# Performance work log

Hardware: AMD Instinct MI355X
Metric: run time of the kernel (lower is better)

The kernel has to match this reference:

```python
import jax, jax.numpy as jnp
import numpy as np

VOC, EDIM, HDIM, SSZ, SDIM, SDEPTH, NACT = 32000, 256, 256, 64, 64, 2, 3
T, B = 256, 128
PAD = 0


def setup_inputs() -> dict:
    key = jax.random.key(0)
    ks = jax.random.split(key, 20)
    s = 0.1
    inp = {
        'inputs': jax.random.randint(ks[0], (T, B), 0, VOC, dtype=jnp.int64) if jax.config.jax_enable_x64 else jax.random.randint(ks[0], (T, B), 0, VOC, dtype=jnp.int32),
        'emb_W': (jax.random.normal(ks[1], (VOC, EDIM)) * s).at[PAD].set(0.0),
        'W_hh': jax.random.normal(ks[2], (HDIM, HDIM)) * s,
        'b_hh': jnp.zeros((HDIM,)),
        'W_eh': jax.random.normal(ks[3], (HDIM, EDIM)) * s,
        'b_eh': jnp.zeros((HDIM,)),
        'W_ha': jax.random.normal(ks[4], (NACT, HDIM)) * s,
        'b_ha': jnp.zeros((NACT,)),
        'W_hg': jax.random.normal(ks[5], (1, HDIM)) * s,
        'b_hg': jnp.zeros((1,)),
        'W_hs': jax.random.normal(ks[6], (SDIM, HDIM)) * s,
        'b_hs': jnp.zeros((SDIM,)),
        'W_sh': jax.random.normal(ks[7], (HDIM, SDIM * SDEPTH)) * s,
        'b_sh': jnp.zeros((HDIM,)),
        'W_su': jax.random.normal(ks[8], (SDIM, SDIM * SDEPTH)) * s,
        'b_su': jnp.zeros((SDIM,)),
        'empty_elem': jax.random.normal(ks[9], (1, SDIM)) * s,
    }
    return inp


def _shift_down(s):  # W_down @ s : row i <- row i-1, row 0 <- 0  (push)
    return jnp.concatenate([jnp.zeros_like(s[:, :1]), s[:, :-1]], axis=1)


def _shift_up(s, k):  # (W_up)^k @ s : row i <- row i+k, tail rows <- 0 (pop)
    return jnp.concatenate([s[:, k:], jnp.zeros_like(s[:, :k])], axis=1)


def reference(inputs, emb_W, W_hh, b_hh, W_eh, b_eh, W_ha, b_ha, W_hg, b_hg,
              W_hs, b_hs, W_sh, b_sh, W_su, b_su, empty_elem):
    bsz = inputs.shape[1]
    embs = emb_W[inputs]                               # [T, B, EDIM]
    hid0 = jnp.zeros((bsz, HDIM), embs.dtype)
    stack0 = jnp.broadcast_to(empty_elem, (bsz, SSZ, SDIM))

    def step(carry, emb):
        hid, stack = carry
        tops = stack[:, :SDEPTH].reshape(bsz, SDEPTH * SDIM)
        mhid = emb @ W_eh.T + b_eh + hid @ W_hh.T + b_hh + tops @ W_sh.T + b_sh
        act_logits = hid @ W_ha.T + b_ha               # [B, 3]
        gamma = 1.0 + jax.nn.softplus(hid @ W_hg.T + b_hg)  # [B, 1]
        act = jax.nn.softmax(act_logits, axis=-1)
        sharp = act ** gamma
        sharp = sharp / (jnp.sum(sharp, axis=-1, keepdims=True) + 1e-16)
        act_chosen = jnp.argmax(sharp, axis=-1)        # topk(k=1)
        p_push = sharp[:, 0][:, None, None]
        p_pop = sharp[:, 1][:, None, None]
        p_noop = sharp[:, 2][:, None, None]
        push_val = jax.nn.relu(hid @ W_hs.T + b_hs)    # [B, SDIM]
        u_val = jax.nn.relu(tops @ W_su.T + b_su)      # [B, SDIM]
        stack_push = _shift_down(stack).at[:, 0].add(push_val)
        stack_pop = _shift_down(_shift_up(stack, SDEPTH)).at[:, 0].add(u_val)
        new_stack = p_push * stack_push + p_pop * stack_pop + p_noop * stack
        new_hid = jax.nn.relu(mhid)
        return (new_hid, new_stack), (new_hid, act_chosen)

    (hid, stack), (outputs, acts) = jax.lax.scan(step, (hid0, stack0), embs)
    return outputs, hid, stack, acts
```

## Files before the change

### kernel.cpp

```cpp
#include <hip/hip_runtime.h>

#define T_STEPS 256
#define BATCH 128

#define WEHT_OFF 0
#define WHHT_OFF 65536
#define WSHT_OFF 131072
#define WHST_OFF 163840
#define WSUT_OFF 180224
#define BC_OFF   188416

#define HID_OFF   8388608
#define STACK_OFF 8421376
#define ACTS_OFF  8945664

#define BAR_LDS() do { \
    asm volatile("s_waitcnt lgkmcnt(0)" ::: "memory"); \
    __builtin_amdgcn_s_barrier(); \
} while (0)

__device__ __forceinline__ float rl(float v, int l) {
    return __int_as_float(__builtin_amdgcn_readlane(__float_as_int(v), l));
}

__global__ __launch_bounds__(256) void prep_kernel(
    const float* __restrict__ W_hh, const float* __restrict__ b_hh,
    const float* __restrict__ W_eh, const float* __restrict__ b_eh,
    const float* __restrict__ W_sh, const float* __restrict__ b_sh,
    const float* __restrict__ W_hs, const float* __restrict__ W_su,
    float* __restrict__ ws)
{
    int idx = blockIdx.x * 256 + threadIdx.x;
    if (idx < 65536) {
        ws[WEHT_OFF + idx] = W_eh[(idx & 255) * 256 + (idx >> 8)];
    } else if (idx < 131072) {
        int k = idx - 65536;
        ws[WHHT_OFF + k] = W_hh[(k & 255) * 256 + (k >> 8)];
    } else if (idx < 163840) {
        int k = idx - 131072;
        ws[WSHT_OFF + k] = W_sh[(k & 255) * 128 + (k >> 8)];
    } else if (idx < 180224) {
        int k = idx - 163840;
        ws[WHST_OFF + k] = W_hs[(k & 63) * 256 + (k >> 6)];
    } else if (idx < 188416) {
        int k = idx - 180224;
        ws[WSUT_OFF + k] = W_su[(k & 63) * 128 + (k >> 6)];
    } else if (idx < 188672) {
        int k = idx - 188416;
        ws[BC_OFF + k] = b_eh[k] + b_hh[k] + b_sh[k];
    }
}

__global__ __launch_bounds__(256) void ex_gemm(
    const int* __restrict__ tokens, const float* __restrict__ emb_W,
    const float* __restrict__ ws, float* __restrict__ outp)
{
    __shared__ __align__(16) float aT[64 * 40];
    __shared__ int tok[32];
    const int t = threadIdx.x;
    const int rg = t >> 6;
    const int c0 = (t & 63) * 4;
    const int R0 = blockIdx.x * 32;
    if (t < 32) tok[t] = tokens[R0 + t];
    __syncthreads();

    float acc[8][4];
#pragma unroll
    for (int r = 0; r < 8; r++)
#pragma unroll
        for (int c = 0; c < 4; c++) acc[r][c] = 0.f;

    for (int e0 = 0; e0 < 256; e0 += 64) {
        {
            int r = t >> 3, seg = t & 7;
            const float* src = emb_W + (size_t)tok[r] * 256 + e0 + seg * 8;
            float4 v0 = *(const float4*)(src);
            float4 v1 = *(const float4*)(src + 4);
            int eb = seg * 8;
            aT[(eb + 0) * 40 + r] = v0.x; aT[(eb + 1) * 40 + r] = v0.y;
            aT[(eb + 2) * 40 + r] = v0.z; aT[(eb + 3) * 40 + r] = v0.w;
            aT[(eb + 4) * 40 + r] = v1.x; aT[(eb + 5) * 40 + r] = v1.y;
            aT[(eb + 6) * 40 + r] = v1.z; aT[(eb + 7) * 40 + r] = v1.w;
        }
        __syncthreads();
        const float* wp = ws + WEHT_OFF + (size_t)e0 * 256 + c0;
#pragma unroll 2
        for (int e = 0; e < 64; e++) {
            float4 wv = *(const float4*)(wp + (size_t)e * 256);
            const float* ar = &aT[e * 40 + rg * 8];
            float4 a0 = *(const float4*)(ar);
            float4 a1 = *(const float4*)(ar + 4);
            acc[0][0] = fmaf(a0.x, wv.x, acc[0][0]); acc[0][1] = fmaf(a0.x, wv.y, acc[0][1]);
            acc[0][2] = fmaf(a0.x, wv.z, acc[0][2]); acc[0][3] = fmaf(a0.x, wv.w, acc[0][3]);
            acc[1][0] = fmaf(a0.y, wv.x, acc[1][0]); acc[1][1] = fmaf(a0.y, wv.y, acc[1][1]);
            acc[1][2] = fmaf(a0.y, wv.z, acc[1][2]); acc[1][3] = fmaf(a0.y, wv.w, acc[1][3]);
            acc[2][0] = fmaf(a0.z, wv.x, acc[2][0]); acc[2][1] = fmaf(a0.z, wv.y, acc[2][1]);
            acc[2][2] = fmaf(a0.z, wv.z, acc[2][2]); acc[2][3] = fmaf(a0.z, wv.w, acc[2][3]);
            acc[3][0] = fmaf(a0.w, wv.x, acc[3][0]); acc[3][1] = fmaf(a0.w, wv.y, acc[3][1]);
            acc[3][2] = fmaf(a0.w, wv.z, acc[3][2]); acc[3][3] = fmaf(a0.w, wv.w, acc[3][3]);
            acc[4][0] = fmaf(a1.x, wv.x, acc[4][0]); acc[4][1] = fmaf(a1.x, wv.y, acc[4][1]);
            acc[4][2] = fmaf(a1.x, wv.z, acc[4][2]); acc[4][3] = fmaf(a1.x, wv.w, acc[4][3]);
            acc[5][0] = fmaf(a1.y, wv.x, acc[5][0]); acc[5][1] = fmaf(a1.y, wv.y, acc[5][1]);
            acc[5][2] = fmaf(a1.y, wv.z, acc[5][2]); acc[5][3] = fmaf(a1.y, wv.w, acc[5][3]);
            acc[6][0] = fmaf(a1.z, wv.x, acc[6][0]); acc[6][1] = fmaf(a1.z, wv.y, acc[6][1]);
            acc[6][2] = fmaf(a1.z, wv.z, acc[6][2]); acc[6][3] = fmaf(a1.z, wv.w, acc[6][3]);
            acc[7][0] = fmaf(a1.w, wv.x, acc[7][0]); acc[7][1] = fmaf(a1.w, wv.y, acc[7][1]);
            acc[7][2] = fmaf(a1.w, wv.z, acc[7][2]); acc[7][3] = fmaf(a1.w, wv.w, acc[7][3]);
        }
        __syncthreads();
    }
    float4 bc4 = *(const float4*)&ws[BC_OFF + c0];
#pragma unroll
    for (int r = 0; r < 8; r++) {
        float4 o;
        o.x = acc[r][0] + bc4.x; o.y = acc[r][1] + bc4.y;
        o.z = acc[r][2] + bc4.z; o.w = acc[r][3] + bc4.w;
        *(float4*)&outp[(size_t)(R0 + rg * 8 + r) * 256 + c0] = o;
    }
}

__attribute__((amdgpu_flat_work_group_size(512, 512)))
__attribute__((amdgpu_waves_per_eu(2, 2)))
__global__ void rnn_scan(
    const float* __restrict__ ws,
    const float* __restrict__ W_ha, const float* __restrict__ b_ha,
    const float* __restrict__ W_hg, const float* __restrict__ b_hg,
    const float* __restrict__ b_hs, const float* __restrict__ b_su,
    const float* __restrict__ empty_elem,
    float* __restrict__ out)
{
    __shared__ __align__(16) float hid[256];
    __shared__ __align__(16) float tops[128];
    __shared__ __align__(16) float partial[8 * 256];
    __shared__ __align__(16) float2 pp2[8 * 64];
    __shared__ __align__(16) float bnd[16 * 64];
    __shared__ __align__(16) float wsu_l[8192];
    __shared__ __align__(16) float whs_l[16384];
    __shared__ __align__(16) float whaL[1024];
    __shared__ __align__(16) float scal[4];

    const int t = threadIdx.x, lane = t & 63, w = t >> 6;
    const int b = blockIdx.x;

    float4 whh[32], wsh[16];
    {
        const float* base = ws + WHHT_OFF + (size_t)(w * 32) * 256 + lane * 4;
#pragma unroll
        for (int e = 0; e < 32; e++) whh[e] = *(const float4*)(base + (size_t)e * 256);
        const float* base2 = ws + WSHT_OFF + (size_t)(w * 16) * 256 + lane * 4;
#pragma unroll
        for (int j = 0; j < 16; j++) wsh[j] = *(const float4*)(base2 + (size_t)j * 256);
    }
#pragma unroll
    for (int e = 0; e < 32; e++)
        asm volatile("" : "+v"(whh[e].x), "+v"(whh[e].y), "+v"(whh[e].z), "+v"(whh[e].w));
#pragma unroll
    for (int j = 0; j < 16; j++)
        asm volatile("" : "+v"(wsh[j].x), "+v"(wsh[j].y), "+v"(wsh[j].z), "+v"(wsh[j].w));

    float bscal = 0.f;
    if (lane == 0 && w < 4) bscal = (w < 3) ? b_ha[w] : b_hg[0];
    float bhs_r = 0.f, bsu_r = 0.f;
    if (w == 0) { bhs_r = b_hs[lane]; bsu_r = b_su[lane]; }

    const float ev = empty_elem[lane];
    float sv[8];
#pragma unroll
    for (int k = 0; k < 8; k++) sv[k] = ev;
    if (t < 256) hid[t] = 0.f;
    if (t < 128) tops[t] = empty_elem[t & 63];
    bnd[(w * 2) * 64 + lane] = ev;
    bnd[(w * 2 + 1) * 64 + lane] = ev;
    for (int i = t; i < 16384; i += 512)
        whs_l[(i >> 8) * 256 + (i & 63) * 4 + ((i >> 6) & 3)] = ws[WHST_OFF + i];
    for (int i = t; i < 8192; i += 512) {
        int j = i >> 6, s = i & 63;
        wsu_l[(j >> 2) * 256 + s * 4 + (j & 3)] = ws[WSUT_OFF + i];
    }
    for (int i = t; i < 1024; i += 512)
        whaL[i] = (i < 768) ? W_ha[i] : W_hg[i - 768];
    __syncthreads();

    const float* slice_ptr = (lane < 32) ? &hid[w * 32 + lane]
                                         : &tops[w * 16 + (lane & 15)];

    float exv = (w >= 4) ? out[(size_t)b * 256 + (t - 256)] : 0.f;

    const float4* whs4 = (const float4*)whs_l;
    const float4* wsu4 = (const float4*)wsu_l;

    for (int ts = 0; ts < T_STEPS; ts++) {
        float exn = 0.f;
        if (w >= 4 && ts + 1 < T_STEPS)
            exn = out[((size_t)(ts + 1) * BATCH + b) * 256 + (t - 256)];

        float halo_lo = (w == 0) ? 0.f : bnd[((w - 1) * 2 + 1) * 64 + lane];
        float halo_hi = (w == 7) ? 0.f : bnd[((w + 1) * 2) * 64 + lane];

        float slice = *slice_ptr;
        float4 acc = make_float4(0.f, 0.f, 0.f, 0.f);
        float accP = 0.f, accU = 0.f;
#pragma unroll
        for (int eb = 0; eb < 8; eb++) {
            float4 sp = whs4[(w * 8 + eb) * 64 + lane];
            float h0 = rl(slice, 4 * eb + 0);
            float h1 = rl(slice, 4 * eb + 1);
            float h2 = rl(slice, 4 * eb + 2);
            float h3 = rl(slice, 4 * eb + 3);
            acc.x = fmaf(whh[eb*4+0].x, h0, acc.x);
            acc.y = fmaf(whh[eb*4+0].y, h0, acc.y);
            acc.z = fmaf(whh[eb*4+0].z, h0, acc.z);
            acc.w = fmaf(whh[eb*4+0].w, h0, acc.w);
            acc.x = fmaf(whh[eb*4+1].x, h1, acc.x);
            acc.y = fmaf(whh[eb*4+1].y, h1, acc.y);
            acc.z = fmaf(whh[eb*4+1].z, h1, acc.z);
            acc.w = fmaf(whh[eb*4+1].w, h1, acc.w);
            acc.x = fmaf(whh[eb*4+2].x, h2, acc.x);
            acc.y = fmaf(whh[eb*4+2].y, h2, acc.y);
            acc.z = fmaf(whh[eb*4+2].z, h2, acc.z);
            acc.w = fmaf(whh[eb*4+2].w, h2, acc.w);
            acc.x = fmaf(whh[eb*4+3].x, h3, acc.x);
            acc.y = fmaf(whh[eb*4+3].y, h3, acc.y);
            acc.z = fmaf(whh[eb*4+3].z, h3, acc.z);
            acc.w = fmaf(whh[eb*4+3].w, h3, acc.w);
            accP = fmaf(sp.x, h0, accP);
            accP = fmaf(sp.y, h1, accP);
            accP = fmaf(sp.z, h2, accP);
            accP = fmaf(sp.w, h3, accP);
        }
#pragma unroll
        for (int jb = 0; jb < 4; jb++) {
            float4 su = wsu4[(w * 4 + jb) * 64 + lane];
            float tv0 = rl(slice, 32 + 4 * jb);
            float tv1 = rl(slice, 32 + 4 * jb + 1);
            float tv2 = rl(slice, 32 + 4 * jb + 2);
            float tv3 = rl(slice, 32 + 4 * jb + 3);
            acc.x = fmaf(wsh[jb*4+0].x, tv0, acc.x);
            acc.y = fmaf(wsh[jb*4+0].y, tv0, acc.y);
            acc.z = fmaf(wsh[jb*4+0].z, tv0, acc.z);
            acc.w = fmaf(wsh[jb*4+0].w, tv0, acc.w);
            acc.x = fmaf(wsh[jb*4+1].x, tv1, acc.x);
            acc.y = fmaf(wsh[jb*4+1].y, tv1, acc.y);
            acc.z = fmaf(wsh[jb*4+1].z, tv1, acc.z);
            acc.w = fmaf(wsh[jb*4+1].w, tv1, acc.w);
            acc.x = fmaf(wsh[jb*4+2].x, tv2, acc.x);
            acc.y = fmaf(wsh[jb*4+2].y, tv2, acc.y);
            acc.z = fmaf(wsh[jb*4+2].z, tv2, acc.z);
            acc.w = fmaf(wsh[jb*4+2].w, tv2, acc.w);
            acc.x = fmaf(wsh[jb*4+3].x, tv3, acc.x);
            acc.y = fmaf(wsh[jb*4+3].y, tv3, acc.y);
            acc.z = fmaf(wsh[jb*4+3].z, tv3, acc.z);
            acc.w = fmaf(wsh[jb*4+3].w, tv3, acc.w);
            accU = fmaf(su.x, tv0, accU);
            accU = fmaf(su.y, tv1, accU);
            accU = fmaf(su.z, tv2, accU);
            accU = fmaf(su.w, tv3, accU);
        }
        *(float4*)&partial[w * 256 + lane * 4] = acc;
        pp2[w * 64 + lane] = make_float2(accP, accU);

        if (w < 4) {
            float bd = 0.f;
#pragma unroll
            for (int k = 0; k < 4; k++)
                bd = fmaf(whaL[w * 256 + k * 64 + lane], hid[k * 64 + lane], bd);
#pragma unroll
            for (int off = 32; off > 0; off >>= 1) bd += __shfl_down(bd, off);
            if (lane == 0) scal[w] = bd + bscal;
        }
        BAR_LDS();

        float pvv = 0.f, uvv = 0.f;
        if (w == 0) {
            float v1 = bhs_r, v2 = bsu_r;
#pragma unroll
            for (int q = 0; q < 8; q++) {
                float2 pq = pp2[q * 64 + lane];
                v1 += pq.x; v2 += pq.y;
            }
            pvv = fmaxf(v1, 0.f);
            uvv = fmaxf(v2, 0.f);
        }

        if (w >= 4) {
            int h = t - 256;
            float mh = exv;
#pragma unroll
            for (int q = 0; q < 8; q++) mh += partial[q * 256 + h];
            float nh = fmaxf(mh, 0.f);
            hid[h] = nh;
            out[((size_t)ts * BATCH + b) * 256 + h] = nh;
        }

        float4 sc4 = *(const float4*)scal;
        float l0 = sc4.x, l1 = sc4.y, l2 = sc4.z, gv = sc4.w;
        float eg = __expf(gv);
        float g = 1.f + ((gv > 15.f) ? gv : __logf(1.f + eg));
        float m = fmaxf(l0, fmaxf(l1, l2));
        float z = __expf(l0 - m) + __expf(l1 - m) + __expf(l2 - m);
        float lz = __logf(z);
        float s0  = __expf(g * (l0 - m - lz));
        float s1v = __expf(g * (l1 - m - lz));
        float s2v = __expf(g * (l2 - m - lz));
        float S = s0 + s1v + s2v + 1e-16f;
        float rS = __builtin_amdgcn_rcpf(S);
        float p0 = s0 * rS, p1 = s1v * rS, p2 = s2v * rS;

        if (t == 0) {
            int am = 0; float bm = s0;
            if (s1v > bm) { bm = s1v; am = 1; }
            if (s2v > bm) { bm = s2v; am = 2; }
            out[ACTS_OFF + ts * BATCH + b] = (float)am;
        }

        {
            float nv[8];
            float below0 = (w == 0) ? pvv : halo_lo;
            float pop0   = (w == 0) ? uvv : sv[1];
            nv[0] = fmaf(p0, below0, fmaf(p1, pop0, p2 * sv[0]));
#pragma unroll
            for (int k = 1; k < 7; k++)
                nv[k] = fmaf(p0, sv[k - 1], fmaf(p1, sv[k + 1], p2 * sv[k]));
            nv[7] = fmaf(p0, sv[6], fmaf(p1, halo_hi, p2 * sv[7]));
#pragma unroll
            for (int k = 0; k < 8; k++) sv[k] = nv[k];
        }
        bnd[(w * 2) * 64 + lane] = sv[0];
        bnd[(w * 2 + 1) * 64 + lane] = sv[7];
        if (w == 0) { tops[lane] = sv[0]; tops[64 + lane] = sv[1]; }

        exv = exn;
        BAR_LDS();
    }

    if (t < 256) out[HID_OFF + (size_t)b * 256 + t] = hid[t];
#pragma unroll
    for (int k = 0; k < 8; k++)
        out[STACK_OFF + (size_t)b * 4096 + (w * 8 + k) * 64 + lane] = sv[k];
}

extern "C" void kernel_launch(void* const* d_in, const int* in_sizes, int n_in,
                              void* d_out, int out_size, void* d_ws, size_t ws_size,
                              hipStream_t stream)
{
    (void)in_sizes; (void)n_in; (void)out_size; (void)ws_size;
    const int*   inputs     = (const int*)d_in[0];
    const float* emb_W      = (const float*)d_in[1];
    const float* W_hh       = (const float*)d_in[2];
    const float* b_hh       = (const float*)d_in[3];
    const float* W_eh       = (const float*)d_in[4];
    const float* b_eh       = (const float*)d_in[5];
    const float* W_ha       = (const float*)d_in[6];
    const float* b_ha       = (const float*)d_in[7];
    const float* W_hg       = (const float*)d_in[8];
    const float* b_hg       = (const float*)d_in[9];
    const float* W_hs       = (const float*)d_in[10];
    const float* b_hs       = (const float*)d_in[11];
    const float* W_sh       = (const float*)d_in[12];
    const float* b_sh       = (const float*)d_in[13];
    const float* W_su       = (const float*)d_in[14];
    const float* b_su       = (const float*)d_in[15];
    const float* empty_elem = (const float*)d_in[16];
    float* out = (float*)d_out;
    float* ws  = (float*)d_ws;

    hipLaunchKernelGGL(prep_kernel, dim3(737), dim3(256), 0, stream,
                       W_hh, b_hh, W_eh, b_eh, W_sh, b_sh, W_hs, W_su, ws);
    hipLaunchKernelGGL(ex_gemm, dim3(1024), dim3(256), 0, stream,
                       inputs, emb_W, ws, out);
    hipLaunchKernelGGL(rnn_scan, dim3(128), dim3(512), 0, stream,
                       ws, W_ha, b_ha, W_hg, b_hg, b_hs, b_su, empty_elem, out);
}
```

Measured before the change: 593.9 us.

## Use packed FMA in scan matvec and readlane-broadcast embeddings in ex_gemm

The recurrent matvec in rnn_scan now keeps its weights as float2 vectors and uses two-wide elementwise FMA, so the compiler can emit v_pk_fma_f32 and halve the FMA instruction count on the serial critical path. ex_gemm drops its LDS transpose staging and barriers: each lane loads one embedding element per row, values are broadcast with readlane, and the accumulation also uses packed FMA. The inner loop is fully unrolled, which raises code size and register pressure. The readlane broadcasts add scalar-path traffic in exchange for removing LDS traffic.

```diff
diff --git a/kernel.cpp b/kernel.cpp
--- a/kernel.cpp
+++ b/kernel.cpp
@@ -13,6 +13,8 @@
 #define HID_OFF   8388608
 #define STACK_OFF 8421376
 #define ACTS_OFF  8945664
+
+typedef __attribute__((ext_vector_type(2))) float f32x2;
 
 #define BAR_LDS() do { \
     asm volatile("s_waitcnt lgkmcnt(0)" ::: "memory"); \
@@ -55,66 +57,48 @@
     const int* __restrict__ tokens, const float* __restrict__ emb_W,
     const float* __restrict__ ws, float* __restrict__ outp)
 {
-    __shared__ __align__(16) float aT[64 * 40];
     __shared__ int tok[32];
-    const int t = threadIdx.x;
-    const int rg = t >> 6;
-    const int c0 = (t & 63) * 4;
+    const int t = threadIdx.x, lane = t & 63, rg = t >> 6;
+    const int c0 = lane * 4;
     const int R0 = blockIdx.x * 32;
     if (t < 32) tok[t] = tokens[R0 + t];
     __syncthreads();
-
-    float acc[8][4];
-#pragma unroll
-    for (int r = 0; r < 8; r++)
-#pragma unroll
-        for (int c = 0; c < 4; c++) acc[r][c] = 0.f;
+    int tr[8];
+#pragma unroll
+    for (int r = 0; r < 8; r++) tr[r] = tok[rg * 8 + r];
+
+    f32x2 accA[8], accB[8];
+#pragma unroll
+    for (int r = 0; r < 8; r++) {
+        accA[r] = (f32x2){0.f, 0.f};
+        accB[r] = (f32x2){0.f, 0.f};
+    }
 
     for (int e0 = 0; e0 < 256; e0 += 64) {
-        {
-            int r = t >> 3, seg = t & 7;
-            const float* src = emb_W + (size_t)tok[r] * 256 + e0 + seg * 8;
-            float4 v0 = *(const float4*)(src);
-            float4 v1 = *(const float4*)(src + 4);
-            int eb = seg * 8;
-            aT[(eb + 0) * 40 + r] = v0.x; aT[(eb + 1) * 40 + r] = v0.y;
-            aT[(eb + 2) * 40 + r] = v0.z; aT[(eb + 3) * 40 + r] = v0.w;
-            aT[(eb + 4) * 40 + r] = v1.x; aT[(eb + 5) * 40 + r] = v1.y;
-            aT[(eb + 6) * 40 + r] = v1.z; aT[(eb + 7) * 40 + r] = v1.w;
-        }
-        __syncthreads();
+        float er[8];
+#pragma unroll
+        for (int r = 0; r < 8; r++)
+            er[r] = emb_W[(size_t)tr[r] * 256 + e0 + lane];
         const float* wp = ws + WEHT_OFF + (size_t)e0 * 256 + c0;
-#pragma unroll 2
+#pragma unroll
         for (int e = 0; e < 64; e++) {
             float4 wv = *(const float4*)(wp + (size_t)e * 256);
-            const float* ar = &aT[e * 40 + rg * 8];
-            float4 a0 = *(const float4*)(ar);
-            float4 a1 = *(const float4*)(ar + 4);
-            acc[0][0] = fmaf(a0.x, wv.x, acc[0][0]); acc[0][1] = fmaf(a0.x, wv.y, acc[0][1]);
-            acc[0][2] = fmaf(a0.x, wv.z, acc[0][2]); acc[0][3] = fmaf(a0.x, wv.w, acc[0][3]);
-            acc[1][0] = fmaf(a0.y, wv.x, acc[1][0]); acc[1][1] = fmaf(a0.y, wv.y, acc[1][1]);
-            acc[1][2] = fmaf(a0.y, wv.z, acc[1][2]); acc[1][3] = fmaf(a0.y, wv.w, acc[1][3]);
-            acc[2][0] = fmaf(a0.z, wv.x, acc[2][0]); acc[2][1] = fmaf(a0.z, wv.y, acc[2][1]);
-            acc[2][2] = fmaf(a0.z, wv.z, acc[2][2]); acc[2][3] = fmaf(a0.z, wv.w, acc[2][3]);
-            acc[3][0] = fmaf(a0.w, wv.x, acc[3][0]); acc[3][1] = fmaf(a0.w, wv.y, acc[3][1]);
-            acc[3][2] = fmaf(a0.w, wv.z, acc[3][2]); acc[3][3] = fmaf(a0.w, wv.w, acc[3][3]);
-            acc[4][0] = fmaf(a1.x, wv.x, acc[4][0]); acc[4][1] = fmaf(a1.x, wv.y, acc[4][1]);
-            acc[4][2] = fmaf(a1.x, wv.z, acc[4][2]); acc[4][3] = fmaf(a1.x, wv.w, acc[4][3]);
-            acc[5][0] = fmaf(a1.y, wv.x, acc[5][0]); acc[5][1] = fmaf(a1.y, wv.y, acc[5][1]);
-            acc[5][2] = fmaf(a1.y, wv.z, acc[5][2]); acc[5][3] = fmaf(a1.y, wv.w, acc[5][3]);
-            acc[6][0] = fmaf(a1.z, wv.x, acc[6][0]); acc[6][1] = fmaf(a1.z, wv.y, acc[6][1]);
-            acc[6][2] = fmaf(a1.z, wv.z, acc[6][2]); acc[6][3] = fmaf(a1.z, wv.w, acc[6][3]);
-            acc[7][0] = fmaf(a1.w, wv.x, acc[7][0]); acc[7][1] = fmaf(a1.w, wv.y, acc[7][1]);
-            acc[7][2] = fmaf(a1.w, wv.z, acc[7][2]); acc[7][3] = fmaf(a1.w, wv.w, acc[7][3]);
-        }
-        __syncthreads();
+            f32x2 w01 = {wv.x, wv.y}, w23 = {wv.z, wv.w};
+#pragma unroll
+            for (int r = 0; r < 8; r++) {
+                float a = rl(er[r], e);
+                f32x2 av = {a, a};
+                accA[r] = __builtin_elementwise_fma(w01, av, accA[r]);
+                accB[r] = __builtin_elementwise_fma(w23, av, accB[r]);
+            }
+        }
     }
     float4 bc4 = *(const float4*)&ws[BC_OFF + c0];
 #pragma unroll
     for (int r = 0; r < 8; r++) {
         float4 o;
-        o.x = acc[r][0] + bc4.x; o.y = acc[r][1] + bc4.y;
-        o.z = acc[r][2] + bc4.z; o.w = acc[r][3] + bc4.w;
+        o.x = accA[r].x + bc4.x; o.y = accA[r].y + bc4.y;
+        o.z = accB[r].x + bc4.z; o.w = accB[r].y + bc4.w;
         *(float4*)&outp[(size_t)(R0 + rg * 8 + r) * 256 + c0] = o;
     }
 }
@@ -142,21 +126,27 @@
     const int t = threadIdx.x, lane = t & 63, w = t >> 6;
     const int b = blockIdx.x;
 
-    float4 whh[32], wsh[16];
+    f32x2 whh2[64], wsh2[32];
     {
         const float* base = ws + WHHT_OFF + (size_t)(w * 32) * 256 + lane * 4;
 #pragma unroll
-        for (int e = 0; e < 32; e++) whh[e] = *(const float4*)(base + (size_t)e * 256);
+        for (int e = 0; e < 32; e++) {
+            float4 v = *(const float4*)(base + (size_t)e * 256);
+            whh2[2 * e]     = (f32x2){v.x, v.y};
+            whh2[2 * e + 1] = (f32x2){v.z, v.w};
+        }
         const float* base2 = ws + WSHT_OFF + (size_t)(w * 16) * 256 + lane * 4;
 #pragma unroll
-        for (int j = 0; j < 16; j++) wsh[j] = *(const float4*)(base2 + (size_t)j * 256);
-    }
-#pragma unroll
-    for (int e = 0; e < 32; e++)
-        asm volatile("" : "+v"(whh[e].x), "+v"(whh[e].y), "+v"(whh[e].z), "+v"(whh[e].w));
-#pragma unroll
-    for (int j = 0; j < 16; j++)
-        asm volatile("" : "+v"(wsh[j].x), "+v"(wsh[j].y), "+v"(wsh[j].z), "+v"(wsh[j].w));
+        for (int j = 0; j < 16; j++) {
+            float4 v = *(const float4*)(base2 + (size_t)j * 256);
+            wsh2[2 * j]     = (f32x2){v.x, v.y};
+            wsh2[2 * j + 1] = (f32x2){v.z, v.w};
+        }
+    }
+#pragma unroll
+    for (int i = 0; i < 64; i++) asm volatile("" : "+v"(whh2[i]));
+#pragma unroll
+    for (int i = 0; i < 32; i++) asm volatile("" : "+v"(wsh2[i]));
 
     float bscal = 0.f;
     if (lane == 0 && w < 4) bscal = (w < 3) ? b_ha[w] : b_hg[0];
@@ -198,7 +188,7 @@
         float halo_hi = (w == 7) ? 0.f : bnd[((w + 1) * 2) * 64 + lane];
 
         float slice = *slice_ptr;
-        float4 acc = make_float4(0.f, 0.f, 0.f, 0.f);
+        f32x2 acc01 = (f32x2){0.f, 0.f}, acc23 = (f32x2){0.f, 0.f};
         float accP = 0.f, accU = 0.f;
 #pragma unroll
         for (int eb = 0; eb < 8; eb++) {
@@ -207,22 +197,15 @@
             float h1 = rl(slice, 4 * eb + 1);
             float h2 = rl(slice, 4 * eb + 2);
             float h3 = rl(slice, 4 * eb + 3);
-            acc.x = fmaf(whh[eb*4+0].x, h0, acc.x);
-            acc.y = fmaf(whh[eb*4+0].y, h0, acc.y);
-            acc.z = fmaf(whh[eb*4+0].z, h0, acc.z);
-            acc.w = fmaf(whh[eb*4+0].w, h0, acc.w);
-            acc.x = fmaf(whh[eb*4+1].x, h1, acc.x);
-            acc.y = fmaf(whh[eb*4+1].y, h1, acc.y);
-            acc.z = fmaf(whh[eb*4+1].z, h1, acc.z);
-            acc.w = fmaf(whh[eb*4+1].w, h1, acc.w);
-            acc.x = fmaf(whh[eb*4+2].x, h2, acc.x);
-            acc.y = fmaf(whh[eb*4+2].y, h2, acc.y);
-            acc.z = fmaf(whh[eb*4+2].z, h2, acc.z);
-            acc.w = fmaf(whh[eb*4+2].w, h2, acc.w);
-            acc.x = fmaf(whh[eb*4+3].x, h3, acc.x);
-            acc.y = fmaf(whh[eb*4+3].y, h3, acc.y);
-            acc.z = fmaf(whh[eb*4+3].z, h3, acc.z);
-            acc.w = fmaf(whh[eb*4+3].w, h3, acc.w);
+            f32x2 h0v = {h0, h0}, h1v = {h1, h1}, h2v = {h2, h2}, h3v = {h3, h3};
+            acc01 = __builtin_elementwise_fma(whh2[(4*eb+0)*2],   h0v, acc01);
+            acc23 = __builtin_elementwise_fma(whh2[(4*eb+0)*2+1], h0v, acc23);
+            acc01 = __builtin_elementwise_fma(whh2[(4*eb+1)*2],   h1v, acc01);
+            acc23 = __builtin_elementwise_fma(whh2[(4*eb+1)*2+1], h1v, acc23);
+            acc01 = __builtin_elementwise_fma(whh2[(4*eb+2)*2],   h2v, acc01);
+            acc23 = __builtin_elementwise_fma(whh2[(4*eb+2)*2+1], h2v, acc23);
+            acc01 = __builtin_elementwise_fma(whh2[(4*eb+3)*2],   h3v, acc01);
+            acc23 = __builtin_elementwise_fma(whh2[(4*eb+3)*2+1], h3v, acc23);
             accP = fmaf(sp.x, h0, accP);
             accP = fmaf(sp.y, h1, accP);
             accP = fmaf(sp.z, h2, accP);
@@ -235,28 +218,22 @@
             float tv1 = rl(slice, 32 + 4 * jb + 1);
             float tv2 = rl(slice, 32 + 4 * jb + 2);
             float tv3 = rl(slice, 32 + 4 * jb + 3);
-            acc.x = fmaf(wsh[jb*4+0].x, tv0, acc.x);
-            acc.y = fmaf(wsh[jb*4+0].y, tv0, acc.y);
-            acc.z = fmaf(wsh[jb*4+0].z, tv0, acc.z);
-            acc.w = fmaf(wsh[jb*4+0].w, tv0, acc.w);
-            acc.x = fmaf(wsh[jb*4+1].x, tv1, acc.x);
-            acc.y = fmaf(wsh[jb*4+1].y, tv1, acc.y);
-            acc.z = fmaf(wsh[jb*4+1].z, tv1, acc.z);
-            acc.w = fmaf(wsh[jb*4+1].w, tv1, acc.w);
-            acc.x = fmaf(wsh[jb*4+2].x, tv2, acc.x);
-            acc.y = fmaf(wsh[jb*4+2].y, tv2, acc.y);
-            acc.z = fmaf(wsh[jb*4+2].z, tv2, acc.z);
-            acc.w = fmaf(wsh[jb*4+2].w, tv2, acc.w);
-            acc.x = fmaf(wsh[jb*4+3].x, tv3, acc.x);
-            acc.y = fmaf(wsh[jb*4+3].y, tv3, acc.y);
-            acc.z = fmaf(wsh[jb*4+3].z, tv3, acc.z);
-            acc.w = fmaf(wsh[jb*4+3].w, tv3, acc.w);
+            f32x2 t0v = {tv0, tv0}, t1v = {tv1, tv1}, t2v = {tv2, tv2}, t3v = {tv3, tv3};
+            acc01 = __builtin_elementwise_fma(wsh2[(4*jb+0)*2],   t0v, acc01);
+            acc23 = __builtin_elementwise_fma(wsh2[(4*jb+0)*2+1], t0v, acc23);
+            acc01 = __builtin_elementwise_fma(wsh2[(4*jb+1)*2],   t1v, acc01);
+            acc23 = __builtin_elementwise_fma(wsh2[(4*jb+1)*2+1], t1v, acc23);
+            acc01 = __builtin_elementwise_fma(wsh2[(4*jb+2)*2],   t2v, acc01);
+            acc23 = __builtin_elementwise_fma(wsh2[(4*jb+2)*2+1], t2v, acc23);
+            acc01 = __builtin_elementwise_fma(wsh2[(4*jb+3)*2],   t3v, acc01);
+            acc23 = __builtin_elementwise_fma(wsh2[(4*jb+3)*2+1], t3v, acc23);
             accU = fmaf(su.x, tv0, accU);
             accU = fmaf(su.y, tv1, accU);
             accU = fmaf(su.z, tv2, accU);
             accU = fmaf(su.w, tv3, accU);
         }
-        *(float4*)&partial[w * 256 + lane * 4] = acc;
+        *(float4*)&partial[w * 256 + lane * 4] =
+            make_float4(acc01.x, acc01.y, acc23.x, acc23.y);
         pp2[w * 64 + lane] = make_float2(accP, accU);
 
         if (w < 4) {
```

Result: faster. 572.6 us (-3.6%).
